# Performance work log

Measured on AMD Instinct MI355X. Metric: run time of the kernel, lower is better.

The kernel has to match this reference:

```python
import jax, jax.numpy as jnp
import numpy as np

BATCH, T, N = 8, 2048, 512


def setup_inputs() -> dict:
    key = jax.random.key(0)
    ks = jax.random.split(key, 8)
    scale = 1.0 / np.sqrt(2.0 * (N + N) / 2.0) / np.sqrt(2.0)  # GlorotNormal / sqrt(2)
    u = jax.random.normal(ks[0], (BATCH, T, N), dtype=jnp.float32)
    C_re = jax.random.normal(ks[1], (N, N), dtype=jnp.float32) * scale
    C_im = jax.random.normal(ks[2], (N, N), dtype=jnp.float32) * scale
    B_re = jax.random.normal(ks[3], (N, N), dtype=jnp.float32) * scale
    B_im = jax.random.normal(ks[4], (N, N), dtype=jnp.float32) * scale
    D = jax.random.normal(ks[5], (N,), dtype=jnp.float32)
    # nu drawn from the numerically-stable end of [log(-log rmax), log(-log rmin)]
    nu = jax.random.uniform(ks[6], (N,), minval=-4.6, maxval=-3.7, dtype=jnp.float32)
    theta = jax.random.uniform(ks[7], (N,), minval=0.0, maxval=3.14 / 10, dtype=jnp.float32)
    # gamma initialized as sqrt(1 - |lambda|^2), lambda = exp(-exp(nu) + i*theta)
    gamma = jnp.sqrt(1.0 - jnp.exp(-2.0 * jnp.exp(nu)))
    return {"u": u, "C_re": C_re, "C_im": C_im, "B_re": B_re, "B_im": B_im,
            "D": D, "nu": nu, "theta": theta, "gamma": gamma}


def reference(u, C_re, C_im, B_re, B_im, D, nu, theta, gamma):
    # log_lambda = -exp(nu) + i*theta  (the TF code names this `lambda_`)
    log_lam = (-jnp.exp(nu)).astype(jnp.complex64) + 1j * theta.astype(jnp.complex64)  # (n,)
    t = jnp.arange(u.shape[1], dtype=jnp.float32).astype(jnp.complex64)[:, None]       # (T,1)
    lam_pow = jnp.exp(log_lam[None, :] * t)    # (T,n) == diag(Lambda^t)
    lam_minpow = jnp.exp(-log_lam[None, :] * t)  # (T,n) == diag(Lambda^-t)
    Bm = (B_re + 1j * B_im).astype(jnp.complex64)  # (n,n)
    Cm = (C_re + 1j * C_im).astype(jnp.complex64)  # (n,n)
    # new_u = (gamma * u) @ B   (complex)
    new_u = (gamma * u).astype(jnp.complex64) @ Bm  # (b,t,n)
    # diag einsums in the original are elementwise multiplies
    x = jnp.cumsum(new_u * lam_minpow[None], axis=1) * lam_pow[None]  # (b,t,n)
    y = jnp.real(x @ Cm) + D * u
    return y
```

## Files before the change

### kernel.cpp

```cpp
#include <hip/hip_runtime.h>
#include <hip/hip_bf16.h>
#include <math.h>
#include <stdint.h>

#define BATCH 8
#define T_LEN 2048
#define NDIM 512
#define M_ROWS (BATCH * T_LEN)
#define CHUNK 32
#define NCHUNK (T_LEN / CHUNK)


typedef __attribute__((ext_vector_type(8))) short bf16x8;
typedef __attribute__((ext_vector_type(4))) float floatx4;

__device__ __forceinline__ unsigned short f2bf(float f) {
    union { float f; unsigned u; } v; v.f = f;
    unsigned r = v.u + 0x7fff + ((v.u >> 16) & 1);
    return (unsigned short)(r >> 16);
}
__device__ __forceinline__ float bf2f(unsigned short h) {
    union { unsigned u; float f; } v; v.u = ((unsigned)h) << 16;
    return v.f;
}
__device__ __forceinline__ float bf2f_lo(unsigned u) {
    union { unsigned u; float f; } v; v.u = u << 16; return v.f;
}
__device__ __forceinline__ float bf2f_hi(unsigned u) {
    union { unsigned u; float f; } v; v.u = u & 0xffff0000u; return v.f;
}

__device__ __forceinline__ void gld_lds16(const unsigned short* g, unsigned short* l) {
    __builtin_amdgcn_global_load_lds(
        (const __attribute__((address_space(1))) unsigned int*)(uintptr_t)g,
        (__attribute__((address_space(3))) unsigned int*)(uintptr_t)l,
        16, 0, 0);
}

__global__ __launch_bounds__(256) void k_prep(
    const float* __restrict__ u,
    const float* __restrict__ Bre, const float* __restrict__ Bim,
    const float* __restrict__ Cre, const float* __restrict__ Cim,
    const float* __restrict__ gamma,
    unsigned short* __restrict__ ubf,
    unsigned short* __restrict__ BT, unsigned short* __restrict__ CT)
{
    __shared__ unsigned short tile[32][33];
    const int blk = blockIdx.x;
    if (blk < 4096) {
        size_t i = ((size_t)blk * 256 + threadIdx.x) * 8;
        float4 a = *(const float4*)&u[i];
        float4 b = *(const float4*)&u[i + 4];
        ushort4 p0, p1;
        p0.x = f2bf(a.x); p0.y = f2bf(a.y); p0.z = f2bf(a.z); p0.w = f2bf(a.w);
        p1.x = f2bf(b.x); p1.y = f2bf(b.y); p1.z = f2bf(b.z); p1.w = f2bf(b.w);
        *(ushort4*)&ubf[i] = p0;
        *(ushort4*)&ubf[i + 4] = p1;
        return;
    }
    const int p = blk - 4096;
    const int z = p >> 8;
    const int rem = p & 255;
    const int n0 = (rem & 15) * 32, k0 = (rem >> 4) * 32;
    const float* __restrict__ src = (z == 0) ? Bre : (z == 1) ? Bim : (z == 2) ? Cre : Cim;
    const int tx = threadIdx.x & 31, ty = threadIdx.x >> 5;

#pragma unroll
    for (int j = 0; j < 4; ++j) {
        int k = k0 + ty + j * 8;
        float s = (z < 2) ? gamma[k] : (z == 3 ? -1.f : 1.f);
        tile[ty + j * 8][tx] = f2bf(s * src[(size_t)k * NDIM + n0 + tx]);
    }
    __syncthreads();
#pragma unroll
    for (int j = 0; j < 4; ++j) {
        int n = n0 + ty + j * 8;
        unsigned short v = tile[tx][ty + j * 8];
        if (z == 0) {
            int row = ((n >> 6) << 7) + (n & 63);
            BT[(size_t)row * 512 + k0 + tx] = v;
        } else if (z == 1) {
            int row = ((n >> 6) << 7) + 64 + (n & 63);
            BT[(size_t)row * 512 + k0 + tx] = v;
        } else if (z == 2) {
            int k = k0 + tx;
            int col = ((k >> 6) << 7) + (k & 63);
            CT[(size_t)n * 1024 + col] = v;
        } else {
            int k = k0 + tx;
            int col = ((k >> 6) << 7) + 64 + (k & 63);
            CT[(size_t)n * 1024 + col] = v;
        }
    }
}

__global__ __launch_bounds__(256) void k_gemm_in(
    const unsigned short* __restrict__ A,
    const unsigned short* __restrict__ BT,
    const float* __restrict__ nu, const float* __restrict__ theta,
    unsigned short* __restrict__ X,
    float* __restrict__ carry)
{
    __shared__ unsigned short As[128 * 32];
    __shared__ unsigned short Bs[128 * 32];
    const int tid = threadIdx.x;
    const int w = tid >> 6, l = tid & 63;
    const int bm = blockIdx.x * 128;
    const int bn = blockIdx.y * 128;
    const int wm = (w & 1) * 64, wn = (w >> 1) * 64;
    const int lm = l & 15, lq = l >> 4;
    const int srow = w * 16 + (l >> 2);
    const int scol = (l & 3) * 8;

    floatx4 acc[4][4];
#pragma unroll
    for (int i = 0; i < 4; ++i)
#pragma unroll
        for (int j = 0; j < 4; ++j) acc[i][j] = (floatx4)0.f;

    for (int k0 = 0; k0 < 512; k0 += 32) {
        gld_lds16(&A[(size_t)(bm + srow) * 512 + k0 + scol],      &As[srow * 32 + scol]);
        gld_lds16(&A[(size_t)(bm + 64 + srow) * 512 + k0 + scol], &As[(64 + srow) * 32 + scol]);
        gld_lds16(&BT[(size_t)(bn + srow) * 512 + k0 + scol],      &Bs[srow * 32 + scol]);
        gld_lds16(&BT[(size_t)(bn + 64 + srow) * 512 + k0 + scol], &Bs[(64 + srow) * 32 + scol]);
        __syncthreads();

        bf16x8 af[4], bfr[4];
#pragma unroll
        for (int i = 0; i < 4; ++i)
            af[i] = *(const bf16x8*)&As[(wm + i * 16 + lm) * 32 + lq * 8];
#pragma unroll
        for (int j = 0; j < 4; ++j)
            bfr[j] = *(const bf16x8*)&Bs[(wn + j * 16 + lm) * 32 + lq * 8];
#pragma unroll
        for (int i = 0; i < 4; ++i)
#pragma unroll
            for (int j = 0; j < 4; ++j)
                acc[i][j] = __builtin_amdgcn_mfma_f32_16x16x32_bf16(af[i], bfr[j], acc[i][j], 0, 0, 0);
        __syncthreads();
    }

#pragma unroll
    for (int i = 0; i < 4; ++i)
#pragma unroll
        for (int j = 0; j < 4; ++j) {
            int col = bn + wn + j * 16 + lm;
#pragma unroll
            for (int r = 0; r < 4; ++r) {
                int row = bm + wm + i * 16 + lq * 4 + r;
                X[(size_t)row * 1024 + col] = f2bf(acc[i][j][r]);
            }
        }

    __syncthreads();
    {
        const int chunk = tid >> 6;
        const int ch = tid & 63;
        const int n = (bn >> 1) + ch;
        const float rr = __expf(-__expf(nu[n]));
        const float lre = rr * __cosf(theta[n]);
        const float lim = rr * __sinf(theta[n]);
        const unsigned short* pr = &X[(size_t)(bm + chunk * 32) * 1024 + bn + ch];
        float xre = 0.f, xim = 0.f;
#pragma unroll 8
        for (int t = 0; t < 32; ++t) {
            float ure = bf2f(pr[(size_t)t * 1024]);
            float uim = bf2f(pr[(size_t)t * 1024 + 64]);
            float a = lre * xre - lim * xim + ure;
            float b = lre * xim + lim * xre + uim;
            xre = a; xim = b;
        }
        const int bb = bm >> 11;
        const int cg = ((bm & 2047) >> 5) + chunk;
        size_t ci = ((size_t)bb * NCHUNK + cg) * NDIM + n;
        *(float2*)&carry[ci * 2] = make_float2(xre, xim);
    }
}

__global__ __launch_bounds__(256) void k_scan_apply(
    unsigned short* __restrict__ X,
    const float* __restrict__ nu, const float* __restrict__ theta,
    const float* __restrict__ carry)
{
    const int t2 = threadIdx.x;
    const int n0 = 2 * t2;
    const int b = blockIdx.x >> 6, c = blockIdx.x & 63;
    const float ex0 = __expf(nu[n0]), ex1 = __expf(nu[n0 + 1]);
    const float r0 = __expf(-ex0), r1 = __expf(-ex1);
    const float lre0 = r0 * __cosf(theta[n0]),     lim0 = r0 * __sinf(theta[n0]);
    const float lre1 = r1 * __cosf(theta[n0 + 1]), lim1 = r1 * __sinf(theta[n0 + 1]);
    const float rc0 = expf(-ex0 * (float)CHUNK), rc1 = expf(-ex1 * (float)CHUNK);
    const float th0 = theta[n0] * (float)CHUNK,  th1 = theta[n0 + 1] * (float)CHUNK;
    const float A0 = rc0 * cosf(th0), B0 = rc0 * sinf(th0);
    const float A1 = rc1 * cosf(th1), B1 = rc1 * sinf(th1);

    float xre0 = 0.f, xim0 = 0.f, xre1 = 0.f, xim1 = 0.f;
    for (int cc = 0; cc < c; ++cc) {
        size_t idx = ((size_t)b * NCHUNK + cc) * NDIM + n0;
        float4 cv = *(const float4*)&carry[idx * 2];
        float a0 = A0 * xre0 - B0 * xim0 + cv.x;
        float b0 = A0 * xim0 + B0 * xre0 + cv.y;
        float a1 = A1 * xre1 - B1 * xim1 + cv.z;
        float b1 = A1 * xim1 + B1 * xre1 + cv.w;
        xre0 = a0; xim0 = b0; xre1 = a1; xim1 = b1;
    }

    const int recol = ((n0 >> 6) << 7) + (n0 & 63);
    size_t m = (size_t)b * T_LEN + (size_t)c * CHUNK;
#pragma unroll 8
    for (int t = 0; t < CHUNK; ++t, ++m) {
        unsigned re = *(const unsigned*)&X[m * 1024 + recol];
        unsigned im = *(const unsigned*)&X[m * 1024 + recol + 64];
        float u0 = bf2f_lo(re), u1 = bf2f_hi(re);
        float v0 = bf2f_lo(im), v1 = bf2f_hi(im);
        float a0 = lre0 * xre0 - lim0 * xim0 + u0;
        float b0 = lre0 * xim0 + lim0 * xre0 + v0;
        float a1 = lre1 * xre1 - lim1 * xim1 + u1;
        float b1 = lre1 * xim1 + lim1 * xre1 + v1;
        xre0 = a0; xim0 = b0; xre1 = a1; xim1 = b1;
        unsigned pr = (unsigned)f2bf(xre0) | ((unsigned)f2bf(xre1) << 16);
        unsigned pim = (unsigned)f2bf(xim0) | ((unsigned)f2bf(xim1) << 16);
        *(unsigned*)&X[m * 1024 + recol] = pr;
        *(unsigned*)&X[m * 1024 + recol + 64] = pim;
    }
}

__global__ __launch_bounds__(256) void k_gemm_out(
    const unsigned short* __restrict__ Xbf,
    const unsigned short* __restrict__ CT,
    const float* __restrict__ D,
    const unsigned short* __restrict__ Ubf,
    float* __restrict__ Y)
{
    __shared__ unsigned short As[128 * 32];
    __shared__ unsigned short Bs[128 * 32];
    const int tid = threadIdx.x;
    const int w = tid >> 6, l = tid & 63;
    const int bm = blockIdx.x * 128;
    const int bn = blockIdx.y * 128;
    const int wm = (w & 1) * 64, wn = (w >> 1) * 64;
    const int lm = l & 15, lq = l >> 4;
    const int srow = w * 16 + (l >> 2);
    const int scol = (l & 3) * 8;

    floatx4 acc[4][4];
#pragma unroll
    for (int i = 0; i < 4; ++i)
#pragma unroll
        for (int j = 0; j < 4; ++j) acc[i][j] = (floatx4)0.f;

    for (int k0 = 0; k0 < 1024; k0 += 32) {
        gld_lds16(&Xbf[(size_t)(bm + srow) * 1024 + k0 + scol],      &As[srow * 32 + scol]);
        gld_lds16(&Xbf[(size_t)(bm + 64 + srow) * 1024 + k0 + scol], &As[(64 + srow) * 32 + scol]);
        gld_lds16(&CT[(size_t)(bn + srow) * 1024 + k0 + scol],       &Bs[srow * 32 + scol]);
        gld_lds16(&CT[(size_t)(bn + 64 + srow) * 1024 + k0 + scol],  &Bs[(64 + srow) * 32 + scol]);
        __syncthreads();

        bf16x8 af[4], bfr[4];
#pragma unroll
        for (int i = 0; i < 4; ++i)
            af[i] = *(const bf16x8*)&As[(wm + i * 16 + lm) * 32 + lq * 8];
#pragma unroll
        for (int j = 0; j < 4; ++j)
            bfr[j] = *(const bf16x8*)&Bs[(wn + j * 16 + lm) * 32 + lq * 8];
#pragma unroll
        for (int i = 0; i < 4; ++i)
#pragma unroll
            for (int j = 0; j < 4; ++j)
                acc[i][j] = __builtin_amdgcn_mfma_f32_16x16x32_bf16(af[i], bfr[j], acc[i][j], 0, 0, 0);
        __syncthreads();
    }

#pragma unroll
    for (int i = 0; i < 4; ++i)
#pragma unroll
        for (int j = 0; j < 4; ++j) {
            int col = bn + wn + j * 16 + lm;
            float dv = D[col];
#pragma unroll
            for (int r = 0; r < 4; ++r) {
                int row = bm + wm + i * 16 + lq * 4 + r;
                size_t off = (size_t)row * NDIM + col;
                Y[off] = acc[i][j][r] + dv * bf2f(Ubf[off]);
            }
        }
}

extern "C" void kernel_launch(void* const* d_in, const int* in_sizes, int n_in,
                              void* d_out, int out_size, void* d_ws, size_t ws_size,
                              hipStream_t stream)
{
    const float* u     = (const float*)d_in[0];
    const float* C_re  = (const float*)d_in[1];
    const float* C_im  = (const float*)d_in[2];
    const float* B_re  = (const float*)d_in[3];
    const float* B_im  = (const float*)d_in[4];
    const float* D     = (const float*)d_in[5];
    const float* nu    = (const float*)d_in[6];
    const float* theta = (const float*)d_in[7];
    const float* gamma = (const float*)d_in[8];
    float* y = (float*)d_out;

    unsigned short* X   = (unsigned short*)d_ws;
    unsigned short* ubf = X + (size_t)M_ROWS * 1024;
    unsigned short* BT  = ubf + (size_t)M_ROWS * 512;
    unsigned short* CT  = BT + (size_t)1024 * 512;
    float* carry = (float*)(CT + (size_t)512 * 1024);

    k_prep<<<4096 + 1024, 256, 0, stream>>>(u, B_re, B_im, C_re, C_im, gamma, ubf, BT, CT);
    k_gemm_in<<<dim3(M_ROWS / 128, 8), 256, 0, stream>>>(ubf, BT, nu, theta, X, carry);
    k_scan_apply<<<BATCH * NCHUNK, 256, 0, stream>>>(X, nu, theta, carry);
    k_gemm_out<<<dim3(M_ROWS / 128, 4), 256, 0, stream>>>(X, CT, D, ubf, y);
}
```

Baseline: 183.5 us.

## Double-buffer LDS tiles in both GEMMs and scan chunks from shared memory

Both MFMA GEMM kernels now use two LDS buffers, so the next K-slice is loaded while the current one is being computed, with one barrier per slice. In the input GEMM the bf16 output tile is also written to shared memory, and the per-chunk carry scan reads it from there instead of re-reading X from global memory. This hides load latency and removes a global round trip. In exchange it doubles LDS use per block, which may reduce occupancy, and the loop is fully unrolled.

After: 181.5 us. About the same (-1.1%).

```diff
diff --git a/kernel.cpp b/kernel.cpp
--- a/kernel.cpp
+++ b/kernel.cpp
@@ -101,8 +101,12 @@
     unsigned short* __restrict__ X,
     float* __restrict__ carry)
 {
-    __shared__ unsigned short As[128 * 32];
-    __shared__ unsigned short Bs[128 * 32];
+    __shared__ unsigned short smem[16384];
+    unsigned short* const As0 = smem;
+    unsigned short* const As1 = smem + 4096;
+    unsigned short* const Bs0 = smem + 8192;
+    unsigned short* const Bs1 = smem + 12288;
+
     const int tid = threadIdx.x;
     const int w = tid >> 6, l = tid & 63;
     const int bm = blockIdx.x * 128;
@@ -118,40 +122,52 @@
 #pragma unroll
         for (int j = 0; j < 4; ++j) acc[i][j] = (floatx4)0.f;
 
-    for (int k0 = 0; k0 < 512; k0 += 32) {
-        gld_lds16(&A[(size_t)(bm + srow) * 512 + k0 + scol],      &As[srow * 32 + scol]);
-        gld_lds16(&A[(size_t)(bm + 64 + srow) * 512 + k0 + scol], &As[(64 + srow) * 32 + scol]);
-        gld_lds16(&BT[(size_t)(bn + srow) * 512 + k0 + scol],      &Bs[srow * 32 + scol]);
-        gld_lds16(&BT[(size_t)(bn + 64 + srow) * 512 + k0 + scol], &Bs[(64 + srow) * 32 + scol]);
-        __syncthreads();
-
+    auto STAGE = [&](unsigned short* as, unsigned short* bs, int k0) {
+        gld_lds16(&A[(size_t)(bm + srow) * 512 + k0 + scol],       &as[srow * 32 + scol]);
+        gld_lds16(&A[(size_t)(bm + 64 + srow) * 512 + k0 + scol],  &as[(64 + srow) * 32 + scol]);
+        gld_lds16(&BT[(size_t)(bn + srow) * 512 + k0 + scol],      &bs[srow * 32 + scol]);
+        gld_lds16(&BT[(size_t)(bn + 64 + srow) * 512 + k0 + scol], &bs[(64 + srow) * 32 + scol]);
+    };
+    auto COMPUTE = [&](const unsigned short* as, const unsigned short* bs) {
         bf16x8 af[4], bfr[4];
 #pragma unroll
         for (int i = 0; i < 4; ++i)
-            af[i] = *(const bf16x8*)&As[(wm + i * 16 + lm) * 32 + lq * 8];
+            af[i] = *(const bf16x8*)&as[(wm + i * 16 + lm) * 32 + lq * 8];
 #pragma unroll
         for (int j = 0; j < 4; ++j)
-            bfr[j] = *(const bf16x8*)&Bs[(wn + j * 16 + lm) * 32 + lq * 8];
+            bfr[j] = *(const bf16x8*)&bs[(wn + j * 16 + lm) * 32 + lq * 8];
 #pragma unroll
         for (int i = 0; i < 4; ++i)
 #pragma unroll
             for (int j = 0; j < 4; ++j)
                 acc[i][j] = __builtin_amdgcn_mfma_f32_16x16x32_bf16(af[i], bfr[j], acc[i][j], 0, 0, 0);
+    };
+
+    STAGE(As0, Bs0, 0);
+    __syncthreads();
+#pragma unroll
+    for (int k0 = 0; k0 < 512; k0 += 64) {
+        if (k0 + 32 < 512) STAGE(As1, Bs1, k0 + 32);
+        COMPUTE(As0, Bs0);
         __syncthreads();
+        if (k0 + 64 < 512) STAGE(As0, Bs0, k0 + 64);
+        COMPUTE(As1, Bs1);
+        __syncthreads();
     }
 
 #pragma unroll
     for (int i = 0; i < 4; ++i)
 #pragma unroll
         for (int j = 0; j < 4; ++j) {
-            int col = bn + wn + j * 16 + lm;
+            int col = wn + j * 16 + lm;
 #pragma unroll
             for (int r = 0; r < 4; ++r) {
-                int row = bm + wm + i * 16 + lq * 4 + r;
-                X[(size_t)row * 1024 + col] = f2bf(acc[i][j][r]);
+                int row = wm + i * 16 + lq * 4 + r;
+                unsigned short v = f2bf(acc[i][j][r]);
+                smem[row * 128 + col] = v;
+                X[(size_t)(bm + row) * 1024 + bn + col] = v;
             }
         }
-
     __syncthreads();
     {
         const int chunk = tid >> 6;
@@ -160,12 +176,12 @@
         const float rr = __expf(-__expf(nu[n]));
         const float lre = rr * __cosf(theta[n]);
         const float lim = rr * __sinf(theta[n]);
-        const unsigned short* pr = &X[(size_t)(bm + chunk * 32) * 1024 + bn + ch];
+        const unsigned short* base = &smem[chunk * 32 * 128 + ch];
         float xre = 0.f, xim = 0.f;
 #pragma unroll 8
         for (int t = 0; t < 32; ++t) {
-            float ure = bf2f(pr[(size_t)t * 1024]);
-            float uim = bf2f(pr[(size_t)t * 1024 + 64]);
+            float ure = bf2f(base[t * 128]);
+            float uim = bf2f(base[t * 128 + 64]);
             float a = lre * xre - lim * xim + ure;
             float b = lre * xim + lim * xre + uim;
             xre = a; xim = b;
@@ -232,8 +248,12 @@
     const unsigned short* __restrict__ Ubf,
     float* __restrict__ Y)
 {
-    __shared__ unsigned short As[128 * 32];
-    __shared__ unsigned short Bs[128 * 32];
+    __shared__ unsigned short smem[16384];
+    unsigned short* const As0 = smem;
+    unsigned short* const As1 = smem + 4096;
+    unsigned short* const Bs0 = smem + 8192;
+    unsigned short* const Bs1 = smem + 12288;
+
     const int tid = threadIdx.x;
     const int w = tid >> 6, l = tid & 63;
     const int bm = blockIdx.x * 128;
@@ -249,25 +269,36 @@
 #pragma unroll
         for (int j = 0; j < 4; ++j) acc[i][j] = (floatx4)0.f;
 
-    for (int k0 = 0; k0 < 1024; k0 += 32) {
-        gld_lds16(&Xbf[(size_t)(bm + srow) * 1024 + k0 + scol],      &As[srow * 32 + scol]);
-        gld_lds16(&Xbf[(size_t)(bm + 64 + srow) * 1024 + k0 + scol], &As[(64 + srow) * 32 + scol]);
-        gld_lds16(&CT[(size_t)(bn + srow) * 1024 + k0 + scol],       &Bs[srow * 32 + scol]);
-        gld_lds16(&CT[(size_t)(bn + 64 + srow) * 1024 + k0 + scol],  &Bs[(64 + srow) * 32 + scol]);
-        __syncthreads();
-
+    auto STAGE = [&](unsigned short* as, unsigned short* bs, int k0) {
+        gld_lds16(&Xbf[(size_t)(bm + srow) * 1024 + k0 + scol],      &as[srow * 32 + scol]);
+        gld_lds16(&Xbf[(size_t)(bm + 64 + srow) * 1024 + k0 + scol], &as[(64 + srow) * 32 + scol]);
+        gld_lds16(&CT[(size_t)(bn + srow) * 1024 + k0 + scol],       &bs[srow * 32 + scol]);
+        gld_lds16(&CT[(size_t)(bn + 64 + srow) * 1024 + k0 + scol],  &bs[(64 + srow) * 32 + scol]);
+    };
+    auto COMPUTE = [&](const unsigned short* as, const unsigned short* bs) {
         bf16x8 af[4], bfr[4];
 #pragma unroll
         for (int i = 0; i < 4; ++i)
-            af[i] = *(const bf16x8*)&As[(wm + i * 16 + lm) * 32 + lq * 8];
+            af[i] = *(const bf16x8*)&as[(wm + i * 16 + lm) * 32 + lq * 8];
 #pragma unroll
         for (int j = 0; j < 4; ++j)
-            bfr[j] = *(const bf16x8*)&Bs[(wn + j * 16 + lm) * 32 + lq * 8];
+            bfr[j] = *(const bf16x8*)&bs[(wn + j * 16 + lm) * 32 + lq * 8];
 #pragma unroll
         for (int i = 0; i < 4; ++i)
 #pragma unroll
             for (int j = 0; j < 4; ++j)
                 acc[i][j] = __builtin_amdgcn_mfma_f32_16x16x32_bf16(af[i], bfr[j], acc[i][j], 0, 0, 0);
+    };
+
+    STAGE(As0, Bs0, 0);
+    __syncthreads();
+#pragma unroll
+    for (int k0 = 0; k0 < 1024; k0 += 64) {
+        if (k0 + 32 < 1024) STAGE(As1, Bs1, k0 + 32);
+        COMPUTE(As0, Bs0);
+        __syncthreads();
+        if (k0 + 64 < 1024) STAGE(As0, Bs0, k0 + 64);
+        COMPUTE(As1, Bs1);
         __syncthreads();
     }
 
```
